# Performance work log

Measured on AMD Instinct MI355X. Metric: run time of the kernel, lower is better.

## Reference

```python
import jax, jax.numpy as jnp
import numpy as np

TOP_K = 2  # Router hardcodes torch.topk(logits, k=2)


def setup_inputs() -> dict:
    key = jax.random.key(0)
    ks = jax.random.split(key, 5)
    B, S, H, I, E = 2, 2048, 1024, 2816, 8
    x = jax.random.normal(ks[0], (B, S, H), dtype=jnp.float32)
    router_w = jax.random.normal(ks[1], (E, H), dtype=jnp.float32) * (1.0 / np.sqrt(H))
    Wg = jax.random.normal(ks[2], (E, I, H), dtype=jnp.float32) * (1.0 / np.sqrt(H))
    Wu = jax.random.normal(ks[3], (E, I, H), dtype=jnp.float32) * (1.0 / np.sqrt(H))
    Wd = jax.random.normal(ks[4], (E, H, I), dtype=jnp.float32) * (1.0 / np.sqrt(I))
    return {"x": x, "router_w": router_w, "Wg": Wg, "Wu": Wu, "Wd": Wd}


def reference(x, router_w, Wg, Wu, Wd):
    B, S, H = x.shape
    E = router_w.shape[0]
    xf = x.reshape(-1, H)  # [T, H], T = B*S

    # Router: logits -> top-2 -> softmax over the selected 2 logits
    logits = xf @ router_w.T                      # [T, E]
    top_vals, top_idx = jax.lax.top_k(logits, TOP_K)  # [T, 2]
    top_w = jax.nn.softmax(top_vals, axis=-1)     # [T, 2]

    # Dense combine weights: combine[t, e] = sum_k top_w[t,k] * (top_idx[t,k] == e)
    combine = jnp.einsum('tke,tk->te', jax.nn.one_hot(top_idx, E, dtype=xf.dtype), top_w)  # [T, E]

    # All-experts SwiGLU FFN (dense grouped GEMM form, eval: dropout is identity)
    g = jnp.einsum('th,eih->eti', xf, Wg)         # [E, T, I]
    u = jnp.einsum('th,eih->eti', xf, Wu)         # [E, T, I]
    h = jax.nn.silu(g) * u                        # [E, T, I]
    y = jnp.einsum('eti,ehi->eth', h, Wd)         # [E, T, H]

    out = jnp.einsum('te,eth->th', combine, y)    # [T, H]
    return out.reshape(B, S, H)
```

## Files before the change

### kernel.cpp

```cpp
#include <hip/hip_runtime.h>
#include <hip/hip_bf16.h>
#include <stdint.h>

#define T_TOK 4096
#define H_DIM 1024
#define I_DIM 2816
#define E_NUM 8
#define BK 64
#define W_ELEMS 23068672
#define CH4 5632
#define TM_MAX 12
#define NG1 (8 * 44 * TM_MAX)

typedef float f32x4 __attribute__((ext_vector_type(4)));
typedef __bf16 bf16x8 __attribute__((ext_vector_type(8)));
typedef __bf16 bf16x4 __attribute__((ext_vector_type(4)));

__device__ __forceinline__ void gload_lds16(const void* g, void* l) {
    __builtin_amdgcn_global_load_lds((const __attribute__((address_space(1))) void*)g,
                                     (__attribute__((address_space(3))) void*)l, 16, 0, 0);
}

__device__ __forceinline__ bf16x8 cvt8(float4 a, float4 b) {
    bf16x8 r;
    r[0] = (__bf16)a.x; r[1] = (__bf16)a.y; r[2] = (__bf16)a.z; r[3] = (__bf16)a.w;
    r[4] = (__bf16)b.x; r[5] = (__bf16)b.y; r[6] = (__bf16)b.z; r[7] = (__bf16)b.w;
    return r;
}

__device__ __forceinline__ bf16x4 cvt4(float4 v) {
    bf16x4 o;
    o[0] = (__bf16)v.x; o[1] = (__bf16)v.y; o[2] = (__bf16)v.z; o[3] = (__bf16)v.w;
    return o;
}

__device__ __forceinline__ void cvt_stride(const float* __restrict__ src,
                                           __bf16* __restrict__ dst, int bb, int tid) {
    const int n8 = W_ELEMS / 8;
    const int gsz = 2048 * 256;
    const float4* s = (const float4*)src;
    int p = bb * 256 + tid;
    for (; p + gsz < n8; p += 2 * gsz) {
        float4 a0 = s[2 * p], a1 = s[2 * p + 1];
        int q = p + gsz;
        float4 b0 = s[2 * q], b1 = s[2 * q + 1];
        ((bf16x8*)dst)[p] = cvt8(a0, a1);
        ((bf16x8*)dst)[q] = cvt8(b0, b1);
    }
    if (p < n8) {
        float4 a0 = s[2 * p], a1 = s[2 * p + 1];
        ((bf16x8*)dst)[p] = cvt8(a0, a1);
    }
}

__device__ __forceinline__ void cvt_chunk4(const float* __restrict__ src,
                                           __bf16* __restrict__ dst, int chunk, int tid) {
    int i = chunk * 1024 + tid * 4;
    float4 v0 = ((const float4*)src)[i];
    float4 v1 = ((const float4*)src)[i + 1];
    float4 v2 = ((const float4*)src)[i + 2];
    float4 v3 = ((const float4*)src)[i + 3];
    ((bf16x8*)dst)[chunk * 512 + tid * 2]     = cvt8(v0, v1);
    ((bf16x8*)dst)[chunk * 512 + tid * 2 + 1] = cvt8(v2, v3);
}

__global__ __launch_bounds__(256) void k_prep(const float* __restrict__ x,
                                              const float* __restrict__ rw,
                                              const float* __restrict__ Wg,
                                              const float* __restrict__ Wu,
                                              __bf16* __restrict__ xbf,
                                              __bf16* __restrict__ wbf,
                                              int* __restrict__ tops,
                                              float* __restrict__ wslot) {
    const int b = blockIdx.x;
    const int tid = threadIdx.x;
    if (b < 2048) { cvt_stride(Wg, wbf, b, tid); return; }
    if (b < 4096) { cvt_stride(Wu, wbf + (size_t)W_ELEMS, b - 2048, tid); return; }

    const int rb = b - 4096;
    const int wid = tid >> 6, lane = tid & 63;
    const int t = rb * 4 + wid;

    float acc[E_NUM];
#pragma unroll
    for (int e = 0; e < E_NUM; ++e) acc[e] = 0.f;

    const float4* x4 = (const float4*)(x + (size_t)t * H_DIM);
    const float4* r4 = (const float4*)rw;
#pragma unroll
    for (int j = 0; j < 4; ++j) {
        float4 xv = x4[j * 64 + lane];
        ((bf16x4*)xbf)[(size_t)t * 256 + j * 64 + lane] = cvt4(xv);
#pragma unroll
        for (int e = 0; e < E_NUM; ++e) {
            float4 wv = r4[e * 256 + j * 64 + lane];
            acc[e] += xv.x * wv.x + xv.y * wv.y + xv.z * wv.z + xv.w * wv.w;
        }
    }
#pragma unroll
    for (int s = 1; s < 64; s <<= 1) {
#pragma unroll
        for (int e = 0; e < E_NUM; ++e) acc[e] += __shfl_xor(acc[e], s, 64);
    }
    if (lane == 0) {
        float best = -1e30f; int be = 0;
#pragma unroll
        for (int e = 0; e < E_NUM; ++e) if (acc[e] > best) { best = acc[e]; be = e; }
        float sec = -1e30f; int se = 0;
#pragma unroll
        for (int e = 0; e < E_NUM; ++e) if (e != be && acc[e] > sec) { sec = acc[e]; se = e; }
        float d = __expf(sec - best);
        tops[t] = be | (se << 8);
        wslot[2 * t] = 1.f / (1.f + d);
        wslot[2 * t + 1] = d / (1.f + d);
    }
}

__global__ __launch_bounds__(64) void k_build(const int* __restrict__ tops,
                                              int* __restrict__ list,
                                              int* __restrict__ counts) {
    const int e = blockIdx.x;
    const int lane = threadIdx.x;
    const unsigned long long ltmask = (1ull << lane) - 1;
    int cnt = 0;

    for (int i = 0; i < T_TOK / 64; ++i) {
        int t = i * 64 + lane;
        int p = tops[t];
        bool h1 = (p & 255) == e;
        bool h2 = ((p >> 8) & 255) == e;
        unsigned long long m1 = __ballot(h1);
        if (h1) list[e * T_TOK + cnt + __popcll(m1 & ltmask)] = 2 * t;
        int n1 = __popcll(m1);
        unsigned long long m2 = __ballot(h2);
        if (h2) list[e * T_TOK + cnt + n1 + __popcll(m2 & ltmask)] = 2 * t + 1;
        cnt += n1 + __popcll(m2);
    }
    if (lane == 0) counts[e] = cnt;
}

__global__ __launch_bounds__(256, 4) void k_gemm1(const __bf16* __restrict__ xbf,
                                                  const __bf16* __restrict__ wbf,
                                                  const float* __restrict__ Wd,
                                                  __bf16* __restrict__ wd_bf,
                                                  const int* __restrict__ list,
                                                  const int* __restrict__ counts,
                                                  __bf16* __restrict__ hbuf) {
    __shared__ __attribute__((aligned(16))) unsigned char lA[128 * 128];
    __shared__ __attribute__((aligned(16))) unsigned char lBg[64 * 128];
    __shared__ __attribute__((aligned(16))) unsigned char lBu[64 * 128];
    __shared__ int slots[128];

    const int lid = blockIdx.x;
    const int tid = threadIdx.x;
    if (lid >= NG1) {
        cvt_chunk4(Wd, wd_bf, lid - NG1, tid);
        return;
    }

    const __bf16* wg = wbf;
    const __bf16* wu = wbf + (size_t)W_ELEMS;

    const int e = lid & 7;
    const int seq = lid >> 3;
    const int tn = seq / TM_MAX;
    const int tm = seq % TM_MAX;
    const int cnt = counts[e];
    if (tm * 128 >= cnt) return;
    const int lane = tid & 63;
    const int wid = tid >> 6;
    const int wm = wid >> 1;
    const int wn = wid & 1;

    if (tid < 128) {
        int p = tm * 128 + tid;
        slots[tid] = list[e * T_TOK + (p < cnt ? p : cnt - 1)];
    }
    __syncthreads();

    const char* aSrc[4];
    uint32_t aOff[4];
    {
        int colb = (tid & 7) * 16;
#pragma unroll
        for (int r = 0; r < 4; ++r) {
            int row = r * 32 + (tid >> 3);
            int tok = slots[row] >> 1;
            aSrc[r] = (const char*)xbf + (size_t)tok * (H_DIM * 2) + (colb ^ ((row & 7) << 4));
            aOff[r] = (uint32_t)(row * 128 + colb);
        }
    }
    const char* bgSrc[2];
    const char* buSrc[2];
    uint32_t bOff[2];
    {
        int colb = (tid & 7) * 16;
#pragma unroll
        for (int r = 0; r < 2; ++r) {
            int row = r * 32 + (tid >> 3);
            size_t gr = ((size_t)e * I_DIM + (size_t)tn * 64 + row) * (H_DIM * 2) + (colb ^ ((row & 7) << 4));
            bgSrc[r] = (const char*)wg + gr;
            buSrc[r] = (const char*)wu + gr;
            bOff[r] = (uint32_t)(row * 128 + colb);
        }
    }

    const f32x4 zero = {0.f, 0.f, 0.f, 0.f};
    f32x4 accg[4][2], accu[4][2];
#pragma unroll
    for (int i = 0; i < 4; ++i)
#pragma unroll
        for (int j = 0; j < 2; ++j) { accg[i][j] = zero; accu[i][j] = zero; }

    const int NT = H_DIM / BK;
    for (int kt = 0; kt < NT; ++kt) {
        if (kt > 0) __syncthreads();
#pragma unroll
        for (int r = 0; r < 4; ++r) gload_lds16(aSrc[r] + kt * 128, &lA[aOff[r]]);
#pragma unroll
        for (int r = 0; r < 2; ++r) {
            gload_lds16(bgSrc[r] + kt * 128, &lBg[bOff[r]]);
            gload_lds16(buSrc[r] + kt * 128, &lBu[bOff[r]]);
        }
        __syncthreads();
        __builtin_amdgcn_s_setprio(1);
#pragma unroll
        for (int kk = 0; kk < 2; ++kk) {
            bf16x8 av[4], bg[2], bu[2];
#pragma unroll
            for (int mi = 0; mi < 4; ++mi) {
                int row = wm * 64 + mi * 16 + (lane & 15);
                int byte = (row * 128 + kk * 64 + (lane >> 4) * 16) ^ ((row & 7) << 4);
                av[mi] = *(const bf16x8*)&lA[byte];
            }
#pragma unroll
            for (int ni = 0; ni < 2; ++ni) {
                int row = wn * 32 + ni * 16 + (lane & 15);
                int byte = (row * 128 + kk * 64 + (lane >> 4) * 16) ^ ((row & 7) << 4);
                bg[ni] = *(const bf16x8*)&lBg[byte];
                bu[ni] = *(const bf16x8*)&lBu[byte];
            }
#pragma unroll
            for (int mi = 0; mi < 4; ++mi)
#pragma unroll
                for (int ni = 0; ni < 2; ++ni) {
                    accg[mi][ni] = __builtin_amdgcn_mfma_f32_16x16x32_bf16(av[mi], bg[ni], accg[mi][ni], 0, 0, 0);
                    accu[mi][ni] = __builtin_amdgcn_mfma_f32_16x16x32_bf16(av[mi], bu[ni], accu[mi][ni], 0, 0, 0);
                }
        }
        __builtin_amdgcn_s_setprio(0);
    }

    __syncthreads();
#pragma unroll
    for (int mi = 0; mi < 4; ++mi)
#pragma unroll
        for (int ni = 0; ni < 2; ++ni)
#pragma unroll
            for (int r = 0; r < 4; ++r) {
                int row = wm * 64 + mi * 16 + ((lane >> 4) << 2) + r;
                int col = wn * 32 + ni * 16 + (lane & 15);
                float g = accg[mi][ni][r];
                float u = accu[mi][ni][r];
                float hv = (g / (1.f + __expf(-g))) * u;
                *(__bf16*)&lA[(row * 128 + col * 2) ^ ((row & 7) << 4)] = (__bf16)hv;
            }
    __syncthreads();
    {
        int row = tid >> 1;
        int half = tid & 1;
        int p = tm * 128 + row;
        if (p < cnt) {
            int slot = slots[row];
            __bf16* dst = hbuf + (size_t)slot * I_DIM + (size_t)tn * 64 + half * 32;
#pragma unroll
            for (int j = 0; j < 4; ++j) {
                bf16x8 v = *(const bf16x8*)&lA[(row * 128 + half * 64 + j * 16) ^ ((row & 7) << 4)];
                *(bf16x8*)(dst + j * 8) = v;
            }
        }
    }
}

__global__ __launch_bounds__(256, 4) void k_gemm2(const __bf16* __restrict__ hbuf,
                                                  const __bf16* __restrict__ wd,
                                                  const int* __restrict__ list,
                                                  const int* __restrict__ counts,
                                                  __bf16* __restrict__ y) {
    __shared__ __attribute__((aligned(16))) unsigned char ldsAB[32768];
    __shared__ int slots[128];
    unsigned char* lA = ldsAB;
    unsigned char* lB = ldsAB + 16384;

    const int lid = blockIdx.x;
    const int e = lid & 7;
    const int seq = lid >> 3;
    const int tn = seq & 7;
    const int kh = (seq >> 3) & 1;
    const int tm = seq >> 4;
    const int cnt = counts[e];
    if (tm * 128 >= cnt) return;
    const int tid = threadIdx.x;
    const int lane = tid & 63;
    const int wid = tid >> 6;
    const int wm = wid >> 1;
    const int wn = wid & 1;

    if (tid < 128) {
        int p = tm * 128 + tid;
        slots[tid] = list[e * T_TOK + (p < cnt ? p : cnt - 1)];
    }
    __syncthreads();

    const int NTH = (I_DIM / BK) / 2;
    const int kbase = kh * NTH;
    __bf16* yh = y + (size_t)kh * (2 * T_TOK) * H_DIM;

    const char* aSrc[4];
    uint32_t aOff[4];
    {
        int colb = (tid & 7) * 16;
#pragma unroll
        for (int r = 0; r < 4; ++r) {
            int row = r * 32 + (tid >> 3);
            aSrc[r] = (const char*)hbuf + (size_t)slots[row] * (I_DIM * 2)
                      + (size_t)kbase * 128 + (colb ^ ((row & 7) << 4));
            aOff[r] = (uint32_t)(row * 128 + colb);
        }
    }
    const char* bSrc[4];
    uint32_t bOff[4];
    {
        int colb = (tid & 7) * 16;
#pragma unroll
        for (int r = 0; r < 4; ++r) {
            int row = r * 32 + (tid >> 3);
            bSrc[r] = (const char*)wd + ((size_t)e * H_DIM + (size_t)tn * 128 + row) * (I_DIM * 2)
                      + (size_t)kbase * 128 + (colb ^ ((row & 7) << 4));
            bOff[r] = (uint32_t)(row * 128 + colb);
        }
    }

    const f32x4 zero = {0.f, 0.f, 0.f, 0.f};
    f32x4 acc[4][4];
#pragma unroll
    for (int i = 0; i < 4; ++i)
#pragma unroll
        for (int j = 0; j < 4; ++j) acc[i][j] = zero;

    for (int kt = 0; kt < NTH; ++kt) {
        if (kt > 0) __syncthreads();
#pragma unroll
        for (int r = 0; r < 4; ++r) {
            gload_lds16(aSrc[r] + kt * 128, &lA[aOff[r]]);
            gload_lds16(bSrc[r] + kt * 128, &lB[bOff[r]]);
        }
        __syncthreads();
        __builtin_amdgcn_s_setprio(1);
#pragma unroll
        for (int kk = 0; kk < 2; ++kk) {
            bf16x8 av[4], bv[4];
#pragma unroll
            for (int mi = 0; mi < 4; ++mi) {
                int row = wm * 64 + mi * 16 + (lane & 15);
                int byte = (row * 128 + kk * 64 + (lane >> 4) * 16) ^ ((row & 7) << 4);
                av[mi] = *(const bf16x8*)&lA[byte];
            }
#pragma unroll
            for (int ni = 0; ni < 4; ++ni) {
                int row = wn * 64 + ni * 16 + (lane & 15);
                int byte = (row * 128 + kk * 64 + (lane >> 4) * 16) ^ ((row & 7) << 4);
                bv[ni] = *(const bf16x8*)&lB[byte];
            }
#pragma unroll
            for (int mi = 0; mi < 4; ++mi)
#pragma unroll
                for (int ni = 0; ni < 4; ++ni)
                    acc[mi][ni] = __builtin_amdgcn_mfma_f32_16x16x32_bf16(av[mi], bv[ni], acc[mi][ni], 0, 0, 0);
        }
        __builtin_amdgcn_s_setprio(0);
    }

    __syncthreads();
#pragma unroll
    for (int mi = 0; mi < 4; ++mi)
#pragma unroll
        for (int ni = 0; ni < 4; ++ni)
#pragma unroll
            for (int r = 0; r < 4; ++r) {
                int row = wm * 64 + mi * 16 + ((lane >> 4) << 2) + r;
                int col = wn * 64 + ni * 16 + (lane & 15);
                *(__bf16*)&ldsAB[(row * 256 + col * 2) ^ ((row & 7) << 4)] = (__bf16)acc[mi][ni][r];
            }
    __syncthreads();
    {
        int row = tid >> 1;
        int half = tid & 1;
        int p = tm * 128 + row;
        if (p < cnt) {
            int slot = slots[row];
            __bf16* dst = yh + (size_t)slot * H_DIM + (size_t)tn * 128 + half * 64;
#pragma unroll
            for (int j = 0; j < 8; ++j) {
                bf16x8 v = *(const bf16x8*)&ldsAB[(row * 256 + half * 128 + j * 16) ^ ((row & 7) << 4)];
                *(bf16x8*)(dst + j * 8) = v;
            }
        }
    }
}

__global__ __launch_bounds__(256) void k_combine(const __bf16* __restrict__ y,
                                                 const float* __restrict__ wslot,
                                                 float* __restrict__ out) {
    const int t = blockIdx.x;
    const int c = threadIdx.x;
    const float w1 = wslot[2 * t];
    const float w2 = wslot[2 * t + 1];
    const size_t half = (size_t)(2 * T_TOK) * H_DIM;
    size_t r1 = (size_t)(2 * t) * H_DIM + c * 4;
    size_t r2 = (size_t)(2 * t + 1) * H_DIM + c * 4;
    bf16x4 a0 = *(const bf16x4*)(y + r1);
    bf16x4 a1 = *(const bf16x4*)(y + r1 + half);
    bf16x4 b0 = *(const bf16x4*)(y + r2);
    bf16x4 b1 = *(const bf16x4*)(y + r2 + half);
    float4 o;
    o.x = w1 * ((float)a0[0] + (float)a1[0]) + w2 * ((float)b0[0] + (float)b1[0]);
    o.y = w1 * ((float)a0[1] + (float)a1[1]) + w2 * ((float)b0[1] + (float)b1[1]);
    o.z = w1 * ((float)a0[2] + (float)a1[2]) + w2 * ((float)b0[2] + (float)b1[2]);
    o.w = w1 * ((float)a0[3] + (float)a1[3]) + w2 * ((float)b0[3] + (float)b1[3]);
    ((float4*)out)[(size_t)t * (H_DIM / 4) + c] = o;
}

extern "C" void kernel_launch(void* const* d_in, const int* in_sizes, int n_in,
                              void* d_out, int out_size, void* d_ws, size_t ws_size,
                              hipStream_t stream) {
    const float* x  = (const float*)d_in[0];
    const float* rw = (const float*)d_in[1];
    const float* Wg = (const float*)d_in[2];
    const float* Wu = (const float*)d_in[3];
    const float* Wd = (const float*)d_in[4];
    float* out = (float*)d_out;

    char* ws = (char*)d_ws;
    const size_t SZ_X = 8388608;
    const size_t SZ_W = 46137344;
    __bf16* xbf   = (__bf16*)(ws);
    __bf16* wbf   = (__bf16*)(ws + SZ_X);
    __bf16* wd_bf = (__bf16*)(ws + SZ_X + 2 * SZ_W);
    __bf16* hbuf  = (__bf16*)(ws + SZ_X + 3 * SZ_W);
    __bf16* y     = (__bf16*)(ws + SZ_X);
    int*    tops  = (int*)hbuf;
    int*    list  = (int*)(ws + SZ_X + 4 * SZ_W);
    float*  wslot = (float*)(ws + SZ_X + 4 * SZ_W + 131072);
    int*    counts= (int*)(ws + SZ_X + 4 * SZ_W + 131072 + 32768);

    k_prep<<<5120, 256, 0, stream>>>(x, rw, Wg, Wu, xbf, wbf, tops, wslot);
    k_build<<<E_NUM, 64, 0, stream>>>(tops, list, counts);
    k_gemm1<<<NG1 + CH4, 256, 0, stream>>>(xbf, wbf, Wd, wd_bf, list, counts, hbuf);
    k_gemm2<<<8 * 8 * 2 * TM_MAX, 256, 0, stream>>>(hbuf, wd_bf, list, counts, y);
    k_combine<<<T_TOK, 256, 0, stream>>>(y, wslot, out);
}
```

Baseline: 299.6 us.

## Double-buffer weight tiles in LDS and prefetch gathered activations into registers

In the gate/up grouped GEMM kernel, activation rows are now loaded directly from global memory into registers in MFMA fragment layout instead of being staged through LDS. Weight tiles are double-buffered in LDS, and the next K tile is prefetched while the current one is multiplied, leaving one barrier per iteration. The goal is to hide global load latency and cut LDS traffic and synchronisation. In exchange it uses more registers, lowers the launch-bounds occupancy target from 4 to 3, and issues uncoalesced per-lane gathers that are duplicated across the two N-waves.

```diff
diff --git a/kernel.cpp b/kernel.cpp
--- a/kernel.cpp
+++ b/kernel.cpp
@@ -139,16 +139,15 @@
     if (lane == 0) counts[e] = cnt;
 }
 
-__global__ __launch_bounds__(256, 4) void k_gemm1(const __bf16* __restrict__ xbf,
+__global__ __launch_bounds__(256, 3) void k_gemm1(const __bf16* __restrict__ xbf,
                                                   const __bf16* __restrict__ wbf,
                                                   const float* __restrict__ Wd,
                                                   __bf16* __restrict__ wd_bf,
                                                   const int* __restrict__ list,
                                                   const int* __restrict__ counts,
                                                   __bf16* __restrict__ hbuf) {
-    __shared__ __attribute__((aligned(16))) unsigned char lA[128 * 128];
-    __shared__ __attribute__((aligned(16))) unsigned char lBg[64 * 128];
-    __shared__ __attribute__((aligned(16))) unsigned char lBu[64 * 128];
+    __shared__ __attribute__((aligned(16))) unsigned char lBg[2][8192];
+    __shared__ __attribute__((aligned(16))) unsigned char lBu[2][8192];
     __shared__ int slots[128];
 
     const int lid = blockIdx.x;
@@ -178,18 +177,6 @@
     }
     __syncthreads();
 
-    const char* aSrc[4];
-    uint32_t aOff[4];
-    {
-        int colb = (tid & 7) * 16;
-#pragma unroll
-        for (int r = 0; r < 4; ++r) {
-            int row = r * 32 + (tid >> 3);
-            int tok = slots[row] >> 1;
-            aSrc[r] = (const char*)xbf + (size_t)tok * (H_DIM * 2) + (colb ^ ((row & 7) << 4));
-            aOff[r] = (uint32_t)(row * 128 + colb);
-        }
-    }
     const char* bgSrc[2];
     const char* buSrc[2];
     uint32_t bOff[2];
@@ -204,6 +191,17 @@
             bOff[r] = (uint32_t)(row * 128 + colb);
         }
     }
+    const char* aB[4];
+    {
+        int rl = lane & 15;
+        int ko = (lane >> 4) * 16;
+#pragma unroll
+        for (int mi = 0; mi < 4; ++mi) {
+            int row = wm * 64 + mi * 16 + rl;
+            int tok = slots[row] >> 1;
+            aB[mi] = (const char*)xbf + (size_t)tok * (H_DIM * 2) + ko;
+        }
+    }
 
     const f32x4 zero = {0.f, 0.f, 0.f, 0.f};
     f32x4 accg[4][2], accu[4][2];
@@ -212,46 +210,65 @@
 #pragma unroll
         for (int j = 0; j < 2; ++j) { accg[i][j] = zero; accu[i][j] = zero; }
 
+    bf16x8 areg[2][4][2];
+
+#pragma unroll
+    for (int r = 0; r < 2; ++r) {
+        gload_lds16(bgSrc[r], &lBg[0][bOff[r]]);
+        gload_lds16(buSrc[r], &lBu[0][bOff[r]]);
+    }
+#pragma unroll
+    for (int mi = 0; mi < 4; ++mi)
+#pragma unroll
+        for (int kk = 0; kk < 2; ++kk)
+            areg[0][mi][kk] = *(const bf16x8*)(aB[mi] + kk * 64);
+    asm volatile("s_waitcnt vmcnt(0)" ::: "memory");
+    __builtin_amdgcn_s_barrier();
+
     const int NT = H_DIM / BK;
+#pragma unroll
     for (int kt = 0; kt < NT; ++kt) {
-        if (kt > 0) __syncthreads();
-#pragma unroll
-        for (int r = 0; r < 4; ++r) gload_lds16(aSrc[r] + kt * 128, &lA[aOff[r]]);
-#pragma unroll
-        for (int r = 0; r < 2; ++r) {
-            gload_lds16(bgSrc[r] + kt * 128, &lBg[bOff[r]]);
-            gload_lds16(buSrc[r] + kt * 128, &lBu[bOff[r]]);
-        }
-        __syncthreads();
-        __builtin_amdgcn_s_setprio(1);
+        const int cur = kt & 1, nxt = cur ^ 1;
+        if (kt + 1 < NT) {
+#pragma unroll
+            for (int r = 0; r < 2; ++r) {
+                gload_lds16(bgSrc[r] + (kt + 1) * 128, &lBg[nxt][bOff[r]]);
+                gload_lds16(buSrc[r] + (kt + 1) * 128, &lBu[nxt][bOff[r]]);
+            }
+#pragma unroll
+            for (int mi = 0; mi < 4; ++mi)
+#pragma unroll
+                for (int kk = 0; kk < 2; ++kk)
+                    areg[nxt][mi][kk] = *(const bf16x8*)(aB[mi] + (kt + 1) * 128 + kk * 64);
+        }
+        __builtin_amdgcn_sched_barrier(0);
 #pragma unroll
         for (int kk = 0; kk < 2; ++kk) {
-            bf16x8 av[4], bg[2], bu[2];
-#pragma unroll
-            for (int mi = 0; mi < 4; ++mi) {
-                int row = wm * 64 + mi * 16 + (lane & 15);
-                int byte = (row * 128 + kk * 64 + (lane >> 4) * 16) ^ ((row & 7) << 4);
-                av[mi] = *(const bf16x8*)&lA[byte];
-            }
+            bf16x8 bg[2], bu[2];
 #pragma unroll
             for (int ni = 0; ni < 2; ++ni) {
                 int row = wn * 32 + ni * 16 + (lane & 15);
                 int byte = (row * 128 + kk * 64 + (lane >> 4) * 16) ^ ((row & 7) << 4);
-                bg[ni] = *(const bf16x8*)&lBg[byte];
-                bu[ni] = *(const bf16x8*)&lBu[byte];
-            }
+                bg[ni] = *(const bf16x8*)&lBg[cur][byte];
+                bu[ni] = *(const bf16x8*)&lBu[cur][byte];
+            }
+            __builtin_amdgcn_s_setprio(1);
 #pragma unroll
             for (int mi = 0; mi < 4; ++mi)
 #pragma unroll
                 for (int ni = 0; ni < 2; ++ni) {
-                    accg[mi][ni] = __builtin_amdgcn_mfma_f32_16x16x32_bf16(av[mi], bg[ni], accg[mi][ni], 0, 0, 0);
-                    accu[mi][ni] = __builtin_amdgcn_mfma_f32_16x16x32_bf16(av[mi], bu[ni], accu[mi][ni], 0, 0, 0);
+                    accg[mi][ni] = __builtin_amdgcn_mfma_f32_16x16x32_bf16(areg[cur][mi][kk], bg[ni], accg[mi][ni], 0, 0, 0);
+                    accu[mi][ni] = __builtin_amdgcn_mfma_f32_16x16x32_bf16(areg[cur][mi][kk], bu[ni], accu[mi][ni], 0, 0, 0);
                 }
-        }
-        __builtin_amdgcn_s_setprio(0);
-    }
-
-    __syncthreads();
+            __builtin_amdgcn_s_setprio(0);
+        }
+        __builtin_amdgcn_sched_barrier(0);
+        if (kt + 1 < NT) { asm volatile("s_waitcnt vmcnt(0)" ::: "memory"); }
+        __builtin_amdgcn_s_barrier();
+        __builtin_amdgcn_sched_barrier(0);
+    }
+
+    unsigned char* sC = &lBg[0][0];
 #pragma unroll
     for (int mi = 0; mi < 4; ++mi)
 #pragma unroll
@@ -263,7 +280,7 @@
                 float g = accg[mi][ni][r];
                 float u = accu[mi][ni][r];
                 float hv = (g / (1.f + __expf(-g))) * u;
-                *(__bf16*)&lA[(row * 128 + col * 2) ^ ((row & 7) << 4)] = (__bf16)hv;
+                *(__bf16*)&sC[(row * 128 + col * 2) ^ ((row & 7) << 4)] = (__bf16)hv;
             }
     __syncthreads();
     {
@@ -275,7 +292,7 @@
             __bf16* dst = hbuf + (size_t)slot * I_DIM + (size_t)tn * 64 + half * 32;
 #pragma unroll
             for (int j = 0; j < 4; ++j) {
-                bf16x8 v = *(const bf16x8*)&lA[(row * 128 + half * 64 + j * 16) ^ ((row & 7) << 4)];
+                bf16x8 v = *(const bf16x8*)&sC[(row * 128 + half * 64 + j * 16) ^ ((row & 7) << 4)];
                 *(bf16x8*)(dst + j * 8) = v;
             }
         }
```

Result: slower. 422.4 us (+41.0%).

## Fuse fp32-to-bf16 weight conversion into GEMM LDS loads

Applied to the files above, without the earlier changes.

Removes the separate passes that convert Wg, Wu and Wd to bf16 in workspace. The GEMM kernels now stream fp32 weights straight into LDS through a wider swizzled layout and convert to bf16 in registers before each MFMA. This drops a full read and write of the converted weights, but it doubles LDS footprint and global bytes per B tile inside the GEMMs and lowers occupancy from 4 to 3 blocks. It also adds conversion ALU work to the inner loop.

```diff
diff --git a/kernel.cpp b/kernel.cpp
--- a/kernel.cpp
+++ b/kernel.cpp
@@ -7,8 +7,6 @@
 #define I_DIM 2816
 #define E_NUM 8
 #define BK 64
-#define W_ELEMS 23068672
-#define CH4 5632
 #define TM_MAX 12
 #define NG1 (8 * 44 * TM_MAX)
 
@@ -34,52 +32,18 @@
     return o;
 }
 
-__device__ __forceinline__ void cvt_stride(const float* __restrict__ src,
-                                           __bf16* __restrict__ dst, int bb, int tid) {
-    const int n8 = W_ELEMS / 8;
-    const int gsz = 2048 * 256;
-    const float4* s = (const float4*)src;
-    int p = bb * 256 + tid;
-    for (; p + gsz < n8; p += 2 * gsz) {
-        float4 a0 = s[2 * p], a1 = s[2 * p + 1];
-        int q = p + gsz;
-        float4 b0 = s[2 * q], b1 = s[2 * q + 1];
-        ((bf16x8*)dst)[p] = cvt8(a0, a1);
-        ((bf16x8*)dst)[q] = cvt8(b0, b1);
-    }
-    if (p < n8) {
-        float4 a0 = s[2 * p], a1 = s[2 * p + 1];
-        ((bf16x8*)dst)[p] = cvt8(a0, a1);
-    }
-}
-
-__device__ __forceinline__ void cvt_chunk4(const float* __restrict__ src,
-                                           __bf16* __restrict__ dst, int chunk, int tid) {
-    int i = chunk * 1024 + tid * 4;
-    float4 v0 = ((const float4*)src)[i];
-    float4 v1 = ((const float4*)src)[i + 1];
-    float4 v2 = ((const float4*)src)[i + 2];
-    float4 v3 = ((const float4*)src)[i + 3];
-    ((bf16x8*)dst)[chunk * 512 + tid * 2]     = cvt8(v0, v1);
-    ((bf16x8*)dst)[chunk * 512 + tid * 2 + 1] = cvt8(v2, v3);
-}
-
-__global__ __launch_bounds__(256) void k_prep(const float* __restrict__ x,
-                                              const float* __restrict__ rw,
-                                              const float* __restrict__ Wg,
-                                              const float* __restrict__ Wu,
-                                              __bf16* __restrict__ xbf,
-                                              __bf16* __restrict__ wbf,
-                                              int* __restrict__ tops,
-                                              float* __restrict__ wslot) {
-    const int b = blockIdx.x;
+__device__ __forceinline__ int bswz(int row) {
+    return ((row & 7) << 5) | ((row & 8) << 1);
+}
+
+__global__ __launch_bounds__(256) void k_router(const float* __restrict__ x,
+                                                const float* __restrict__ rw,
+                                                __bf16* __restrict__ xbf,
+                                                int* __restrict__ tops,
+                                                float* __restrict__ wslot) {
     const int tid = threadIdx.x;
-    if (b < 2048) { cvt_stride(Wg, wbf, b, tid); return; }
-    if (b < 4096) { cvt_stride(Wu, wbf + (size_t)W_ELEMS, b - 2048, tid); return; }
-
-    const int rb = b - 4096;
     const int wid = tid >> 6, lane = tid & 63;
-    const int t = rb * 4 + wid;
+    const int t = blockIdx.x * 4 + wid;
 
     float acc[E_NUM];
 #pragma unroll
@@ -139,27 +103,19 @@
     if (lane == 0) counts[e] = cnt;
 }
 
-__global__ __launch_bounds__(256, 4) void k_gemm1(const __bf16* __restrict__ xbf,
-                                                  const __bf16* __restrict__ wbf,
-                                                  const float* __restrict__ Wd,
-                                                  __bf16* __restrict__ wd_bf,
+__global__ __launch_bounds__(256, 3) void k_gemm1(const __bf16* __restrict__ xbf,
+                                                  const float* __restrict__ Wg,
+                                                  const float* __restrict__ Wu,
                                                   const int* __restrict__ list,
                                                   const int* __restrict__ counts,
                                                   __bf16* __restrict__ hbuf) {
-    __shared__ __attribute__((aligned(16))) unsigned char lA[128 * 128];
-    __shared__ __attribute__((aligned(16))) unsigned char lBg[64 * 128];
-    __shared__ __attribute__((aligned(16))) unsigned char lBu[64 * 128];
+    __shared__ __attribute__((aligned(16))) unsigned char lA[16384];
+    __shared__ __attribute__((aligned(16))) unsigned char lBg[16384];
+    __shared__ __attribute__((aligned(16))) unsigned char lBu[16384];
     __shared__ int slots[128];
 
     const int lid = blockIdx.x;
     const int tid = threadIdx.x;
-    if (lid >= NG1) {
-        cvt_chunk4(Wd, wd_bf, lid - NG1, tid);
-        return;
-    }
-
-    const __bf16* wg = wbf;
-    const __bf16* wu = wbf + (size_t)W_ELEMS;
 
     const int e = lid & 7;
     const int seq = lid >> 3;
@@ -190,18 +146,18 @@
             aOff[r] = (uint32_t)(row * 128 + colb);
         }
     }
-    const char* bgSrc[2];
-    const char* buSrc[2];
-    uint32_t bOff[2];
-    {
-        int colb = (tid & 7) * 16;
-#pragma unroll
-        for (int r = 0; r < 2; ++r) {
-            int row = r * 32 + (tid >> 3);
-            size_t gr = ((size_t)e * I_DIM + (size_t)tn * 64 + row) * (H_DIM * 2) + (colb ^ ((row & 7) << 4));
-            bgSrc[r] = (const char*)wg + gr;
-            buSrc[r] = (const char*)wu + gr;
-            bOff[r] = (uint32_t)(row * 128 + colb);
+    const char* bgSrc[4];
+    const char* buSrc[4];
+    uint32_t bOff[4];
+    {
+        int inner = (tid & 15) * 16;
+#pragma unroll
+        for (int r = 0; r < 4; ++r) {
+            int row = r * 16 + (tid >> 4);
+            size_t gr = ((size_t)e * I_DIM + (size_t)tn * 64 + row) * (H_DIM * 4) + (inner ^ bswz(row));
+            bgSrc[r] = (const char*)Wg + gr;
+            buSrc[r] = (const char*)Wu + gr;
+            bOff[r] = (uint32_t)(row * 256 + inner);
         }
     }
 
@@ -218,9 +174,9 @@
 #pragma unroll
         for (int r = 0; r < 4; ++r) gload_lds16(aSrc[r] + kt * 128, &lA[aOff[r]]);
 #pragma unroll
-        for (int r = 0; r < 2; ++r) {
-            gload_lds16(bgSrc[r] + kt * 128, &lBg[bOff[r]]);
-            gload_lds16(buSrc[r] + kt * 128, &lBu[bOff[r]]);
+        for (int r = 0; r < 4; ++r) {
+            gload_lds16(bgSrc[r] + kt * 256, &lBg[bOff[r]]);
+            gload_lds16(buSrc[r] + kt * 256, &lBu[bOff[r]]);
         }
         __syncthreads();
         __builtin_amdgcn_s_setprio(1);
@@ -236,9 +192,14 @@
 #pragma unroll
             for (int ni = 0; ni < 2; ++ni) {
                 int row = wn * 32 + ni * 16 + (lane & 15);
-                int byte = (row * 128 + kk * 64 + (lane >> 4) * 16) ^ ((row & 7) << 4);
-                bg[ni] = *(const bf16x8*)&lBg[byte];
-                bu[ni] = *(const bf16x8*)&lBu[byte];
+                int base = row * 256 + kk * 128 + (lane >> 4) * 32;
+                int s = bswz(row);
+                float4 g0 = *(const float4*)&lBg[base ^ s];
+                float4 g1 = *(const float4*)&lBg[(base + 16) ^ s];
+                float4 u0 = *(const float4*)&lBu[base ^ s];
+                float4 u1 = *(const float4*)&lBu[(base + 16) ^ s];
+                bg[ni] = cvt8(g0, g1);
+                bu[ni] = cvt8(u0, u1);
             }
 #pragma unroll
             for (int mi = 0; mi < 4; ++mi)
@@ -263,7 +224,7 @@
                 float g = accg[mi][ni][r];
                 float u = accu[mi][ni][r];
                 float hv = (g / (1.f + __expf(-g))) * u;
-                *(__bf16*)&lA[(row * 128 + col * 2) ^ ((row & 7) << 4)] = (__bf16)hv;
+                *(__bf16*)&lBg[(row * 128 + col * 2) ^ ((row & 7) << 4)] = (__bf16)hv;
             }
     __syncthreads();
     {
@@ -275,19 +236,19 @@
             __bf16* dst = hbuf + (size_t)slot * I_DIM + (size_t)tn * 64 + half * 32;
 #pragma unroll
             for (int j = 0; j < 4; ++j) {
-                bf16x8 v = *(const bf16x8*)&lA[(row * 128 + half * 64 + j * 16) ^ ((row & 7) << 4)];
+                bf16x8 v = *(const bf16x8*)&lBg[(row * 128 + half * 64 + j * 16) ^ ((row & 7) << 4)];
                 *(bf16x8*)(dst + j * 8) = v;
             }
         }
     }
 }
 
-__global__ __launch_bounds__(256, 4) void k_gemm2(const __bf16* __restrict__ hbuf,
-                                                  const __bf16* __restrict__ wd,
+__global__ __launch_bounds__(256, 3) void k_gemm2(const __bf16* __restrict__ hbuf,
+                                                  const float* __restrict__ Wd,
                                                   const int* __restrict__ list,
                                                   const int* __restrict__ counts,
                                                   __bf16* __restrict__ y) {
-    __shared__ __attribute__((aligned(16))) unsigned char ldsAB[32768];
+    __shared__ __attribute__((aligned(16))) unsigned char ldsAB[49152];
     __shared__ int slots[128];
     unsigned char* lA = ldsAB;
     unsigned char* lB = ldsAB + 16384;
@@ -328,16 +289,16 @@
             aOff[r] = (uint32_t)(row * 128 + colb);
         }
     }
-    const char* bSrc[4];
-    uint32_t bOff[4];
-    {
-        int colb = (tid & 7) * 16;
-#pragma unroll
-        for (int r = 0; r < 4; ++r) {
-            int row = r * 32 + (tid >> 3);
-            bSrc[r] = (const char*)wd + ((size_t)e * H_DIM + (size_t)tn * 128 + row) * (I_DIM * 2)
-                      + (size_t)kbase * 128 + (colb ^ ((row & 7) << 4));
-            bOff[r] = (uint32_t)(row * 128 + colb);
+    const char* bSrc[8];
+    uint32_t bOff[8];
+    {
+        int inner = (tid & 15) * 16;
+#pragma unroll
+        for (int r = 0; r < 8; ++r) {
+            int row = r * 16 + (tid >> 4);
+            bSrc[r] = (const char*)Wd + ((size_t)e * H_DIM + (size_t)tn * 128 + row) * (I_DIM * 4)
+                      + (size_t)kbase * 256 + (inner ^ bswz(row));
+            bOff[r] = (uint32_t)(row * 256 + inner);
         }
     }
 
@@ -351,10 +312,9 @@
     for (int kt = 0; kt < NTH; ++kt) {
         if (kt > 0) __syncthreads();
 #pragma unroll
-        for (int r = 0; r < 4; ++r) {
-            gload_lds16(aSrc[r] + kt * 128, &lA[aOff[r]]);
-            gload_lds16(bSrc[r] + kt * 128, &lB[bOff[r]]);
-        }
+        for (int r = 0; r < 4; ++r) gload_lds16(aSrc[r] + kt * 128, &lA[aOff[r]]);
+#pragma unroll
+        for (int r = 0; r < 8; ++r) gload_lds16(bSrc[r] + kt * 256, &lB[bOff[r]]);
         __syncthreads();
         __builtin_amdgcn_s_setprio(1);
 #pragma unroll
@@ -369,8 +329,11 @@
 #pragma unroll
             for (int ni = 0; ni < 4; ++ni) {
                 int row = wn * 64 + ni * 16 + (lane & 15);
-                int byte = (row * 128 + kk * 64 + (lane >> 4) * 16) ^ ((row & 7) << 4);
-                bv[ni] = *(const bf16x8*)&lB[byte];
+                int base = row * 256 + kk * 128 + (lane >> 4) * 32;
+                int s = bswz(row);
+                float4 b0 = *(const float4*)&lB[base ^ s];
+                float4 b1 = *(const float4*)&lB[(base + 16) ^ s];
+                bv[ni] = cvt8(b0, b1);
             }
 #pragma unroll
             for (int mi = 0; mi < 4; ++mi)
@@ -443,20 +406,19 @@
 
     char* ws = (char*)d_ws;
     const size_t SZ_X = 8388608;
-    const size_t SZ_W = 46137344;
+    const size_t SZ_H = 46137344;
+    const size_t SZ_Y = 33554432;
     __bf16* xbf   = (__bf16*)(ws);
-    __bf16* wbf   = (__bf16*)(ws + SZ_X);
-    __bf16* wd_bf = (__bf16*)(ws + SZ_X + 2 * SZ_W);
-    __bf16* hbuf  = (__bf16*)(ws + SZ_X + 3 * SZ_W);
-    __bf16* y     = (__bf16*)(ws + SZ_X);
+    __bf16* hbuf  = (__bf16*)(ws + SZ_X);
+    __bf16* y     = (__bf16*)(ws + SZ_X + SZ_H);
     int*    tops  = (int*)hbuf;
-    int*    list  = (int*)(ws + SZ_X + 4 * SZ_W);
-    float*  wslot = (float*)(ws + SZ_X + 4 * SZ_W + 131072);
-    int*    counts= (int*)(ws + SZ_X + 4 * SZ_W + 131072 + 32768);
-
-    k_prep<<<5120, 256, 0, stream>>>(x, rw, Wg, Wu, xbf, wbf, tops, wslot);
+    int*    list  = (int*)(ws + SZ_X + SZ_H + SZ_Y);
+    float*  wslot = (float*)(ws + SZ_X + SZ_H + SZ_Y + 131072);
+    int*    counts= (int*)(ws + SZ_X + SZ_H + SZ_Y + 131072 + 32768);
+
+    k_router<<<T_TOK / 4, 256, 0, stream>>>(x, rw, xbf, tops, wslot);
     k_build<<<E_NUM, 64, 0, stream>>>(tops, list, counts);
-    k_gemm1<<<NG1 + CH4, 256, 0, stream>>>(xbf, wbf, Wd, wd_bf, list, counts, hbuf);
-    k_gemm2<<<8 * 8 * 2 * TM_MAX, 256, 0, stream>>>(hbuf, wd_bf, list, counts, y);
+    k_gemm1<<<NG1, 256, 0, stream>>>(xbf, Wg, Wu, list, counts, hbuf);
+    k_gemm2<<<8 * 8 * 2 * TM_MAX, 256, 0, stream>>>(hbuf, Wd, list, counts, y);
     k_combine<<<T_TOK, 256, 0, stream>>>(y, wslot, out);
 }
```

Result: slower. 322.8 us (+7.8%).
